# Kernel tuning notes

Hardware: AMD Instinct MI355X
Metric: run time of the kernel (lower is better)

Reference implementation:

```python
import jax, jax.numpy as jnp
import numpy as np

N_ART = 50000
N_COMM = 50000
F_IN = 768
PROJ = 1024
HID = 256
OUT = 128


def _sage(x_src, x_dst, ei, Wl, bl, Wr):
    # PyG SAGEConv (aggr='mean', root_weight=True): lin_l(mean_j x_j) + lin_r(x_dst)
    src, dst = ei[0], ei[1]
    n_dst = x_dst.shape[0]
    msg = x_src[src]                                   # [E, d_src] gather
    agg = jax.ops.segment_sum(msg, dst, num_segments=n_dst)
    cnt = jax.ops.segment_sum(jnp.ones((ei.shape[1],), x_src.dtype), dst, num_segments=n_dst)
    mean = agg / jnp.maximum(cnt, 1.0)[:, None]
    return mean @ Wl + bl + x_dst @ Wr


def setup_inputs() -> dict:
    key = jax.random.key(0)
    ks = jax.random.split(key, 22)
    w = lambda k, s: (jax.random.normal(k, s, jnp.float32) * 0.02)
    inp = {
        "article_x": jax.random.normal(ks[0], (N_ART, F_IN), jnp.float32),
        "community_x": jax.random.normal(ks[1], (N_COMM, F_IN), jnp.float32),
        "e_wb": jax.random.randint(ks[2], (2, 200000), 0, N_COMM, jnp.int32),
        "e_mb": jax.random.randint(ks[3], (2, 200000), 0, N_COMM, jnp.int32),
        "e_int": jax.random.randint(ks[4], (2, 500000), 0, N_COMM, jnp.int32),
        # lin1 / lin2 projections (F_IN -> PROJ)
        "W1": w(ks[5], (F_IN, PROJ)), "b1": jnp.zeros((PROJ,), jnp.float32),
        "W2": w(ks[6], (F_IN, PROJ)), "b2": jnp.zeros((PROJ,), jnp.float32),
        # conv1: src dim PROJ, dst dim PROJ -> HID
        "Wl1": w(ks[7], (PROJ, HID)), "bl1": jnp.zeros((HID,), jnp.float32), "Wr1": w(ks[8], (PROJ, HID)),
        # conv2: src dim PROJ, dst dim HID -> HID
        "Wl2": w(ks[9], (PROJ, HID)), "bl2": jnp.zeros((HID,), jnp.float32), "Wr2": w(ks[10], (HID, HID)),
        # conv3: src dim HID, dst dim F_IN (raw community.x) -> HID
        "Wl3": w(ks[11], (HID, HID)), "bl3": jnp.zeros((HID,), jnp.float32), "Wr3": w(ks[12], (F_IN, HID)),
        # lin3: HID -> OUT
        "W3": w(ks[13], (HID, OUT)), "b3": jnp.zeros((OUT,), jnp.float32),
    }
    return inp


def reference(article_x, community_x, e_wb, e_mb, e_int,
              W1, b1, W2, b2,
              Wl1, bl1, Wr1, Wl2, bl2, Wr2, Wl3, bl3, Wr3,
              W3, b3):
    ax = article_x @ W1 + b1          # [N_art, PROJ]
    cx = community_x @ W2 + b2        # [N_comm, PROJ]
    h1 = jax.nn.relu(_sage(ax, cx, e_wb, Wl1, bl1, Wr1))            # [N_comm, HID]
    h2 = jax.nn.relu(_sage(ax, h1, e_mb, Wl2, bl2, Wr2))            # [N_comm, HID]
    h3 = jax.nn.relu(_sage(h2, community_x, e_int, Wl3, bl3, Wr3))  # [N_comm, HID]
    return h3 @ W3 + b3               # [N_comm, OUT]
```

## Files before the change

### kernel.cpp

```cpp
#include <hip/hip_runtime.h>
#include <hip/hip_bf16.h>

#define N_NODES 50000
#define M_PAD   50048
#define MT_     391
#define F_IN    768
#define PROJ    1024
#define HID     256
#define OUTD    128
#define E_WB    200000
#define E_MB    200000
#define E_INT   500000

typedef float f32x4 __attribute__((ext_vector_type(4)));
typedef __bf16 bf16x8 __attribute__((ext_vector_type(8)));

__device__ __forceinline__ float bf2f(unsigned short u) {
  union { unsigned int i; float f; } x; x.i = ((unsigned int)u) << 16; return x.f;
}
__device__ __forceinline__ unsigned short f2bf(float f) {
  union { float f; unsigned int i; } x; x.f = f;
  unsigned int r = x.i + 0x7fff + ((x.i >> 16) & 1);
  return (unsigned short)(r >> 16);
}

__device__ __forceinline__ void gl_lds16(const void* g, void* l) {
  __builtin_amdgcn_global_load_lds((const __attribute__((address_space(1))) void*)g,
                                   (__attribute__((address_space(3))) void*)l, 16, 0, 0);
}

__global__ void bias_prep_kernel(const float* __restrict__ b1, const float* __restrict__ b2,
                                 const float* __restrict__ bl1,
                                 const float* __restrict__ Wl1, const float* __restrict__ Wl2,
                                 const float* __restrict__ Wr1,
                                 float* __restrict__ gb1, float* __restrict__ gb2,
                                 float* __restrict__ bv1) {
  int j = threadIdx.x;
  int out = blockIdx.x >> 3;
  int pg = blockIdx.x & 7;
  const float* vb = (out == 2) ? b2 : b1;
  const float* W = (out == 0) ? Wl1 : (out == 1 ? Wl2 : Wr1);
  float s = 0.f;
  int p0 = pg * 128;
#pragma unroll 4
  for (int p = p0; p < p0 + 128; ++p) s += vb[p] * W[p * HID + j];
  if (out == 2 && pg == 0) s += bl1[j];
  float* dst = (out == 0) ? gb1 : (out == 1 ? gb2 : bv1);
  atomicAdd(&dst[j], s);
}

__global__ void tcast_kernel(const float* __restrict__ src, unsigned short* __restrict__ dst,
                             int R, int C) {
  __shared__ float tile[32][33];
  int x = blockIdx.x * 32 + threadIdx.x;
  int y0 = blockIdx.y * 32;
  for (int i = threadIdx.y; i < 32; i += blockDim.y)
    tile[i][threadIdx.x] = src[(long long)(y0 + i) * C + x];
  __syncthreads();
  int xo = blockIdx.y * 32 + threadIdx.x;
  int yo0 = blockIdx.x * 32;
  for (int i = threadIdx.y; i < 32; i += blockDim.y)
    dst[(long long)(yo0 + i) * R + xo] = f2bf(tile[threadIdx.x][i]);
}

__global__ void cast_pad_kernel(const float* __restrict__ src, unsigned short* __restrict__ dst,
                                int rows_valid, long long total_chunks, int cpr) {
  long long i = (long long)blockIdx.x * 256 + threadIdx.x;
  if (i >= total_chunks) return;
  int row = (int)(i / cpr);
  int c8 = (int)(i % cpr);
  uint4 o;
  if (row < rows_valid) {
    const float4* s4 = (const float4*)src;
    long long base = (long long)row * (cpr * 2) + c8 * 2;
    float4 a = s4[base], b = s4[base + 1];
    o.x = (unsigned int)f2bf(a.x) | ((unsigned int)f2bf(a.y) << 16);
    o.y = (unsigned int)f2bf(a.z) | ((unsigned int)f2bf(a.w) << 16);
    o.z = (unsigned int)f2bf(b.x) | ((unsigned int)f2bf(b.y) << 16);
    o.w = (unsigned int)f2bf(b.z) | ((unsigned int)f2bf(b.w) << 16);
  } else {
    o.x = o.y = o.z = o.w = 0u;
  }
  ((uint4*)dst)[i] = o;
}

__global__ void count_all_kernel(const int* __restrict__ dwb, const int* __restrict__ dmb,
                                 const int* __restrict__ dint,
                                 int* __restrict__ cwb, int* __restrict__ cmb,
                                 int* __restrict__ cint) {
  int i = blockIdx.x * blockDim.x + threadIdx.x;
  const int total = E_WB + E_MB + E_INT;
  if (i >= total) return;
  if (i < E_WB) atomicAdd(&cwb[dwb[i]], 1);
  else if (i < E_WB + E_MB) atomicAdd(&cmb[dmb[i - E_WB]], 1);
  else atomicAdd(&cint[dint[i - E_WB - E_MB]], 1);
}

__global__ void scan3_kernel(const int* __restrict__ c0, const int* __restrict__ c1,
                             const int* __restrict__ c2,
                             int* __restrict__ o0, int* __restrict__ o1, int* __restrict__ o2) {
  const int* cnt = blockIdx.x == 0 ? c0 : (blockIdx.x == 1 ? c1 : c2);
  int* off = blockIdx.x == 0 ? o0 : (blockIdx.x == 1 ? o1 : o2);
  const int n = N_NODES;
  __shared__ int part[1024];
  int t = threadIdx.x;
  const int chunk = (n + 1023) / 1024;
  int lo = t * chunk, hi = lo + chunk; if (hi > n) hi = n; if (lo > n) lo = n;
  int s = 0;
  for (int i = lo; i < hi; ++i) s += cnt[i];
  part[t] = s; __syncthreads();
  for (int d = 1; d < 1024; d <<= 1) {
    int v = part[t];
    if (t >= d) v += part[t - d];
    __syncthreads();
    part[t] = v;
    __syncthreads();
  }
  int run = (t == 0) ? 0 : part[t - 1];
  for (int i = lo; i < hi; ++i) { off[i] = run; run += cnt[i]; }
  if (t == 1023) off[n] = part[1023];
}

__global__ void fill_all_kernel(const int* __restrict__ ewb, const int* __restrict__ emb,
                                const int* __restrict__ eint,
                                const int* __restrict__ owb, const int* __restrict__ omb,
                                const int* __restrict__ oint,
                                int* __restrict__ curwb, int* __restrict__ curmb,
                                int* __restrict__ curint,
                                int* __restrict__ swb, int* __restrict__ smb,
                                int* __restrict__ sint) {
  int i = blockIdx.x * blockDim.x + threadIdx.x;
  const int total = E_WB + E_MB + E_INT;
  if (i >= total) return;
  if (i < E_WB) {
    int s = ewb[i], d = ewb[E_WB + i];
    int p = atomicAdd(&curwb[d], 1);
    swb[owb[d] + p] = s;
  } else if (i < E_WB + E_MB) {
    int e = i - E_WB;
    int s = emb[e], d = emb[E_MB + e];
    int p = atomicAdd(&curmb[d], 1);
    smb[omb[d] + p] = s;
  } else {
    int e = i - E_WB - E_MB;
    int s = eint[e], d = eint[E_INT + e];
    int p = atomicAdd(&curint[d], 1);
    sint[oint[d] + p] = s;
  }
}

template <int EPI>
__global__ void __launch_bounds__(256, 2)
gemm_bt_kernel(const unsigned short* __restrict__ A, const unsigned short* __restrict__ BT,
               void* __restrict__ Cv, int K, int N, int Mvalid,
               const float* __restrict__ bias, const unsigned short* __restrict__ addm,
               int addm_stride) {
  __shared__ __align__(16) unsigned short lA[128 * 32];
  __shared__ __align__(16) unsigned short lB[128 * 32];
  const int tid = threadIdx.x;
  const int lane = tid & 63;
  const int wave = tid >> 6;
  const int NT = N >> 7;
  const int mt = blockIdx.x / NT;
  const int nt = blockIdx.x % NT;
  const int m0 = mt * 128, n0 = nt * 128;
  const int wm = (wave & 1) * 64, wn = (wave >> 1) * 64;

  f32x4 acc[4][4];
#pragma unroll
  for (int i = 0; i < 4; ++i)
#pragma unroll
    for (int j = 0; j < 4; ++j)
#pragma unroll
      for (int r = 0; r < 4; ++r) acc[i][j][r] = 0.f;

  const int r0 = tid >> 2;
  const int c0 = (tid & 3) * 8;
  const uint4* A4 = (const uint4*)A;
  const uint4* B4 = (const uint4*)BT;
  const int K8 = K >> 3;
  const int mrow = lane & 15, kq = lane >> 4;
  unsigned short* lAw = &lA[wave * 512];
  unsigned short* lBw = &lB[wave * 512];

  for (int kt = 0; kt < K; kt += 32) {
    const int kc = (kt + c0) >> 3;
    __syncthreads();
    gl_lds16(&A4[(long long)(m0 + r0) * K8 + kc], lAw);
    gl_lds16(&A4[(long long)(m0 + 64 + r0) * K8 + kc], lAw + 2048);
    gl_lds16(&B4[(long long)(n0 + r0) * K8 + kc], lBw);
    gl_lds16(&B4[(long long)(n0 + 64 + r0) * K8 + kc], lBw + 2048);
    __syncthreads();
    bf16x8 af[4], bfr[4];
#pragma unroll
    for (int i = 0; i < 4; ++i) af[i] = *(const bf16x8*)&lA[(wm + i * 16 + mrow) * 32 + kq * 8];
#pragma unroll
    for (int j = 0; j < 4; ++j) bfr[j] = *(const bf16x8*)&lB[(wn + j * 16 + mrow) * 32 + kq * 8];
#pragma unroll
    for (int i = 0; i < 4; ++i)
#pragma unroll
      for (int j = 0; j < 4; ++j)
        acc[i][j] = __builtin_amdgcn_mfma_f32_16x16x32_bf16(af[i], bfr[j], acc[i][j], 0, 0, 0);
  }

  const int col_l = lane & 15, rq = lane >> 4;
#pragma unroll
  for (int i = 0; i < 4; ++i) {
#pragma unroll
    for (int j = 0; j < 4; ++j) {
#pragma unroll
      for (int r = 0; r < 4; ++r) {
        int R = m0 + wm + i * 16 + rq * 4 + r;
        int Cc = n0 + wn + j * 16 + col_l;
        if (R < Mvalid) {
          float v = acc[i][j][r];
          if constexpr (EPI == 0) {
            ((unsigned short*)Cv)[(long long)R * N + Cc] = f2bf(v);
          } else if constexpr (EPI == 1) {
            v += bias[Cc] + bf2f(addm[(long long)R * addm_stride + Cc]);
            v = v > 0.f ? v : 0.f;
            ((unsigned short*)Cv)[(long long)R * N + Cc] = f2bf(v);
          } else {
            ((float*)Cv)[(long long)R * N + Cc] = v + bias[Cc];
          }
        }
      }
    }
  }
}

template <int MODE>
__global__ void agg_kernel(const unsigned short* __restrict__ S, int s_stride,
                           const int* __restrict__ off, const int* __restrict__ srcl,
                           const float* __restrict__ gb, const float* __restrict__ bvec,
                           const unsigned short* __restrict__ addm, int a_stride,
                           unsigned short* __restrict__ out) {
  int d = blockIdx.x;
  int c = threadIdx.x * 4;
  if (d >= N_NODES) {
    ushort4 z; z.x = z.y = z.z = z.w = 0;
    *(ushort4*)&out[(long long)d * HID + c] = z;
    return;
  }
  int lo = off[d], hi = off[d + 1];
  float s0 = 0.f, s1 = 0.f, s2 = 0.f, s3 = 0.f;
  for (int i = lo; i < hi; ++i) {
    int sidx = srcl[i];
    uint2 v = *(const uint2*)&S[(long long)sidx * s_stride + c];
    s0 += bf2f((unsigned short)(v.x & 0xffff));
    s1 += bf2f((unsigned short)(v.x >> 16));
    s2 += bf2f((unsigned short)(v.y & 0xffff));
    s3 += bf2f((unsigned short)(v.y >> 16));
  }
  int deg = hi - lo;
  float inv = deg > 0 ? 1.f / (float)deg : 0.f;
  float v0 = s0 * inv, v1 = s1 * inv, v2 = s2 * inv, v3 = s3 * inv;
  if constexpr (MODE != 2) {
    float g = deg > 0 ? 1.f : 0.f;
    uint2 am = *(const uint2*)&addm[(long long)d * a_stride + c];
    v0 += g * gb[c] + bvec[c] + bf2f((unsigned short)(am.x & 0xffff));
    v1 += g * gb[c + 1] + bvec[c + 1] + bf2f((unsigned short)(am.x >> 16));
    v2 += g * gb[c + 2] + bvec[c + 2] + bf2f((unsigned short)(am.y & 0xffff));
    v3 += g * gb[c + 3] + bvec[c + 3] + bf2f((unsigned short)(am.y >> 16));
    v0 = fmaxf(v0, 0.f); v1 = fmaxf(v1, 0.f); v2 = fmaxf(v2, 0.f); v3 = fmaxf(v3, 0.f);
  }
  ushort4 o;
  o.x = f2bf(v0); o.y = f2bf(v1); o.z = f2bf(v2); o.w = f2bf(v3);
  *(ushort4*)&out[(long long)d * HID + c] = o;
}

extern "C" void kernel_launch(void* const* d_in, const int* in_sizes, int n_in,
                              void* d_out, int out_size, void* d_ws, size_t ws_size,
                              hipStream_t stream) {
  const float* article_x = (const float*)d_in[0];
  const float* community_x = (const float*)d_in[1];
  const int* e_wb = (const int*)d_in[2];
  const int* e_mb = (const int*)d_in[3];
  const int* e_int = (const int*)d_in[4];
  const float* W1 = (const float*)d_in[5];
  const float* b1 = (const float*)d_in[6];
  const float* W2 = (const float*)d_in[7];
  const float* b2 = (const float*)d_in[8];
  const float* Wl1 = (const float*)d_in[9];
  const float* bl1 = (const float*)d_in[10];
  const float* Wr1 = (const float*)d_in[11];
  const float* Wl2 = (const float*)d_in[12];
  const float* bl2 = (const float*)d_in[13];
  const float* Wr2 = (const float*)d_in[14];
  const float* Wl3 = (const float*)d_in[15];
  const float* bl3 = (const float*)d_in[16];
  const float* Wr3 = (const float*)d_in[17];
  const float* W3 = (const float*)d_in[18];
  const float* b3 = (const float*)d_in[19];

  char* base = (char*)d_ws;
  size_t off = 0;
  auto alloc = [&](size_t bytes) -> void* {
    void* r = base + off;
    off += (bytes + 255) & ~(size_t)255;
    return r;
  };

  unsigned short* Xa = (unsigned short*)alloc((size_t)M_PAD * F_IN * 2);
  unsigned short* Xc = (unsigned short*)alloc((size_t)M_PAD * F_IN * 2);
  unsigned short* AP = (unsigned short*)alloc((size_t)M_PAD * 512 * 2);
  unsigned short* CR = (unsigned short*)alloc((size_t)M_PAD * 512 * 2);
  unsigned short* h1bf = (unsigned short*)alloc((size_t)M_PAD * HID * 2);
  unsigned short* HR2 = (unsigned short*)alloc((size_t)M_PAD * HID * 2);
  unsigned short* h2bf = (unsigned short*)alloc((size_t)M_PAD * HID * 2);
  unsigned short* mean3bf = (unsigned short*)alloc((size_t)M_PAD * HID * 2);
  unsigned short* h3bf = (unsigned short*)alloc((size_t)M_PAD * HID * 2);
  unsigned short* W1bf = (unsigned short*)alloc((size_t)F_IN * PROJ * 2);
  unsigned short* W2bf = (unsigned short*)alloc((size_t)F_IN * PROJ * 2);
  unsigned short* WlT = (unsigned short*)alloc((size_t)512 * PROJ * 2);
  unsigned short* Wr1T = (unsigned short*)alloc((size_t)HID * PROJ * 2);
  unsigned short* F12T = (unsigned short*)alloc((size_t)512 * F_IN * 2);
  unsigned short* GT = (unsigned short*)alloc((size_t)512 * F_IN * 2);
  unsigned short* Wr2T = (unsigned short*)alloc((size_t)HID * HID * 2);
  unsigned short* Wl3T = (unsigned short*)alloc((size_t)HID * HID * 2);
  unsigned short* W3T = (unsigned short*)alloc((size_t)OUTD * HID * 2);
  float* gb1 = (float*)alloc(HID * 4);
  float* gb2 = (float*)alloc(HID * 4);
  float* bv1 = (float*)alloc(HID * 4);
  int* ints_base = (int*)alloc((size_t)6 * N_NODES * 4);
  int* cnt_wb = ints_base;
  int* cur_wb = ints_base + N_NODES;
  int* cnt_mb = ints_base + 2 * N_NODES;
  int* cur_mb = ints_base + 3 * N_NODES;
  int* cnt_int = ints_base + 4 * N_NODES;
  int* cur_int = ints_base + 5 * N_NODES;
  int* off_wb = (int*)alloc((size_t)(N_NODES + 1) * 4);
  int* off_mb = (int*)alloc((size_t)(N_NODES + 1) * 4);
  int* off_int = (int*)alloc((size_t)(N_NODES + 1) * 4);
  int* srcl_wb = (int*)alloc((size_t)E_WB * 4);
  int* srcl_mb = (int*)alloc((size_t)E_MB * 4);
  int* srcl_int = (int*)alloc((size_t)E_INT * 4);

  hipMemsetAsync(ints_base, 0, (size_t)6 * N_NODES * 4, stream);
  hipMemsetAsync(gb1, 0, 3 * 1024, stream);

  cast_pad_kernel<<<(F_IN * PROJ / 8 + 255) / 256, 256, 0, stream>>>(W1, W1bf, F_IN, F_IN * (PROJ / 8), PROJ / 8);
  cast_pad_kernel<<<(F_IN * PROJ / 8 + 255) / 256, 256, 0, stream>>>(W2, W2bf, F_IN, F_IN * (PROJ / 8), PROJ / 8);
  tcast_kernel<<<dim3(HID / 32, PROJ / 32), dim3(32, 8), 0, stream>>>(Wl1, WlT, PROJ, HID);
  tcast_kernel<<<dim3(HID / 32, PROJ / 32), dim3(32, 8), 0, stream>>>(Wl2, WlT + 256 * PROJ, PROJ, HID);
  tcast_kernel<<<dim3(HID / 32, PROJ / 32), dim3(32, 8), 0, stream>>>(Wr1, Wr1T, PROJ, HID);
  tcast_kernel<<<dim3(HID / 32, F_IN / 32), dim3(32, 8), 0, stream>>>(Wr3, GT + 256 * F_IN, F_IN, HID);
  tcast_kernel<<<dim3(8, 8), dim3(32, 8), 0, stream>>>(Wr2, Wr2T, HID, HID);
  tcast_kernel<<<dim3(8, 8), dim3(32, 8), 0, stream>>>(Wl3, Wl3T, HID, HID);
  tcast_kernel<<<dim3(4, 8), dim3(32, 8), 0, stream>>>(W3, W3T, HID, OUTD);
  bias_prep_kernel<<<24, 256, 0, stream>>>(b1, b2, bl1, Wl1, Wl2, Wr1, gb1, gb2, bv1);

  gemm_bt_kernel<0><<<4 * 6, 256, 0, stream>>>(WlT, W1bf, F12T, PROJ, F_IN, 512, nullptr, nullptr, 0);
  gemm_bt_kernel<0><<<2 * 6, 256, 0, stream>>>(Wr1T, W2bf, GT, PROJ, F_IN, 256, nullptr, nullptr, 0);

  long long tc = (long long)M_PAD * (F_IN / 8);
  cast_pad_kernel<<<(unsigned)((tc + 255) / 256), 256, 0, stream>>>(article_x, Xa, N_NODES, tc, F_IN / 8);
  cast_pad_kernel<<<(unsigned)((tc + 255) / 256), 256, 0, stream>>>(community_x, Xc, N_NODES, tc, F_IN / 8);

  const int etot = E_WB + E_MB + E_INT;
  count_all_kernel<<<(etot + 255) / 256, 256, 0, stream>>>(e_wb + E_WB, e_mb + E_MB, e_int + E_INT,
                                                           cnt_wb, cnt_mb, cnt_int);
  scan3_kernel<<<3, 1024, 0, stream>>>(cnt_wb, cnt_mb, cnt_int, off_wb, off_mb, off_int);
  fill_all_kernel<<<(etot + 255) / 256, 256, 0, stream>>>(e_wb, e_mb, e_int, off_wb, off_mb, off_int,
                                                          cur_wb, cur_mb, cur_int,
                                                          srcl_wb, srcl_mb, srcl_int);

  gemm_bt_kernel<0><<<MT_ * 4, 256, 0, stream>>>(Xa, F12T, AP, F_IN, 512, N_NODES, nullptr, nullptr, 0);
  gemm_bt_kernel<0><<<MT_ * 4, 256, 0, stream>>>(Xc, GT, CR, F_IN, 512, N_NODES, nullptr, nullptr, 0);

  agg_kernel<0><<<M_PAD, 64, 0, stream>>>(AP, 512, off_wb, srcl_wb, gb1, bv1, CR, 512, h1bf);

  gemm_bt_kernel<0><<<MT_ * 2, 256, 0, stream>>>(h1bf, Wr2T, HR2, HID, HID, N_NODES, nullptr, nullptr, 0);
  agg_kernel<1><<<M_PAD, 64, 0, stream>>>(AP + 256, 512, off_mb, srcl_mb, gb2, bl2, HR2, 256, h2bf);

  agg_kernel<2><<<M_PAD, 64, 0, stream>>>(h2bf, 256, off_int, srcl_int, nullptr, nullptr, nullptr, 0, mean3bf);
  gemm_bt_kernel<1><<<MT_ * 2, 256, 0, stream>>>(mean3bf, Wl3T, h3bf, HID, HID, N_NODES, bl3, CR + 256, 512);

  gemm_bt_kernel<2><<<MT_ * 1, 256, 0, stream>>>(h3bf, W3T, d_out, HID, OUTD, N_NODES, b3, nullptr, 0);

  (void)in_sizes; (void)n_in; (void)out_size; (void)ws_size;
}
```

Before: 935.3 us.

## Merge prep kernels, batch node GEMMs, double K-step per barrier, pack agg blocks

Merges the many weight cast, transpose and bias-prep launches into one prep kernel, and folds both node feature casts into a single launch. The two weight-folding GEMMs and the two big node projection GEMMs are each batched into one launch by picking the B matrix per M tile, and the memsets are combined. The GEMM now stages two 32-wide K slices per barrier pair (64 K per iteration), which halves synchronisation but doubles LDS use. The aggregation kernels pack four destination nodes per 256-thread block instead of one per 64-thread block.

```diff
diff --git a/kernel.cpp b/kernel.cpp
--- a/kernel.cpp
+++ b/kernel.cpp
@@ -11,6 +11,7 @@
 #define E_WB    200000
 #define E_MB    200000
 #define E_INT   500000
+#define BIGM    (1 << 30)
 
 typedef float f32x4 __attribute__((ext_vector_type(4)));
 typedef __bf16 bf16x8 __attribute__((ext_vector_type(8)));
@@ -29,15 +30,66 @@
                                    (__attribute__((address_space(3))) void*)l, 16, 0, 0);
 }
 
-__global__ void bias_prep_kernel(const float* __restrict__ b1, const float* __restrict__ b2,
-                                 const float* __restrict__ bl1,
-                                 const float* __restrict__ Wl1, const float* __restrict__ Wl2,
-                                 const float* __restrict__ Wr1,
-                                 float* __restrict__ gb1, float* __restrict__ gb2,
-                                 float* __restrict__ bv1) {
+__device__ __forceinline__ void dev_cast8(const float* __restrict__ src,
+                                          unsigned short* __restrict__ dst, int blk) {
+  int i = blk * 256 + threadIdx.x;
+  const float4* s4 = (const float4*)src;
+  float4 a = s4[(long long)i * 2], b = s4[(long long)i * 2 + 1];
+  uint4 o;
+  o.x = (unsigned int)f2bf(a.x) | ((unsigned int)f2bf(a.y) << 16);
+  o.y = (unsigned int)f2bf(a.z) | ((unsigned int)f2bf(a.w) << 16);
+  o.z = (unsigned int)f2bf(b.x) | ((unsigned int)f2bf(b.y) << 16);
+  o.w = (unsigned int)f2bf(b.z) | ((unsigned int)f2bf(b.w) << 16);
+  ((uint4*)dst)[i] = o;
+}
+
+__device__ __forceinline__ void dev_tcast(const float* __restrict__ src,
+                                          unsigned short* __restrict__ dst,
+                                          int R, int C, int blk, float (*tile)[33]) {
+  int bx = blk % (C / 32), by = blk / (C / 32);
+  int tx = threadIdx.x & 31, ty = threadIdx.x >> 5;
+  int x = bx * 32 + tx, y0 = by * 32;
+  for (int i = ty; i < 32; i += 8) tile[i][tx] = src[(long long)(y0 + i) * C + x];
+  __syncthreads();
+  int xo = by * 32 + tx, yo0 = bx * 32;
+  for (int i = ty; i < 32; i += 8) dst[(long long)(yo0 + i) * R + xo] = f2bf(tile[tx][i]);
+}
+
+__global__ void prep_all_kernel(const float* __restrict__ W1, const float* __restrict__ W2,
+                                const float* __restrict__ Wl1, const float* __restrict__ Wl2,
+                                const float* __restrict__ Wr1, const float* __restrict__ Wr2,
+                                const float* __restrict__ Wl3, const float* __restrict__ Wr3,
+                                const float* __restrict__ W3,
+                                const float* __restrict__ b1, const float* __restrict__ b2,
+                                const float* __restrict__ bl1,
+                                unsigned short* __restrict__ W1bf, unsigned short* __restrict__ W2bf,
+                                unsigned short* __restrict__ WlT, unsigned short* __restrict__ Wr1T,
+                                unsigned short* __restrict__ GT_wr3, unsigned short* __restrict__ Wr2T,
+                                unsigned short* __restrict__ Wl3T, unsigned short* __restrict__ W3T,
+                                float* __restrict__ gb1, float* __restrict__ gb2,
+                                float* __restrict__ bv1) {
+  __shared__ float tile[32][33];
+  int b = blockIdx.x;
+  if (b < 384) { dev_cast8(W1, W1bf, b); return; }
+  b -= 384;
+  if (b < 384) { dev_cast8(W2, W2bf, b); return; }
+  b -= 384;
+  if (b < 256) { dev_tcast(Wl1, WlT, PROJ, HID, b, tile); return; }
+  b -= 256;
+  if (b < 256) { dev_tcast(Wl2, WlT + 256 * PROJ, PROJ, HID, b, tile); return; }
+  b -= 256;
+  if (b < 256) { dev_tcast(Wr1, Wr1T, PROJ, HID, b, tile); return; }
+  b -= 256;
+  if (b < 192) { dev_tcast(Wr3, GT_wr3, F_IN, HID, b, tile); return; }
+  b -= 192;
+  if (b < 64) { dev_tcast(Wr2, Wr2T, HID, HID, b, tile); return; }
+  b -= 64;
+  if (b < 64) { dev_tcast(Wl3, Wl3T, HID, HID, b, tile); return; }
+  b -= 64;
+  if (b < 32) { dev_tcast(W3, W3T, HID, OUTD, b, tile); return; }
+  b -= 32;
   int j = threadIdx.x;
-  int out = blockIdx.x >> 3;
-  int pg = blockIdx.x & 7;
+  int out = b >> 3, pg = b & 7;
   const float* vb = (out == 2) ? b2 : b1;
   const float* W = (out == 0) ? Wl1 : (out == 1 ? Wl2 : Wr1);
   float s = 0.f;
@@ -49,35 +101,22 @@
   atomicAdd(&dst[j], s);
 }
 
-__global__ void tcast_kernel(const float* __restrict__ src, unsigned short* __restrict__ dst,
-                             int R, int C) {
-  __shared__ float tile[32][33];
-  int x = blockIdx.x * 32 + threadIdx.x;
-  int y0 = blockIdx.y * 32;
-  for (int i = threadIdx.y; i < 32; i += blockDim.y)
-    tile[i][threadIdx.x] = src[(long long)(y0 + i) * C + x];
-  __syncthreads();
-  int xo = blockIdx.y * 32 + threadIdx.x;
-  int yo0 = blockIdx.x * 32;
-  for (int i = threadIdx.y; i < 32; i += blockDim.y)
-    dst[(long long)(yo0 + i) * R + xo] = f2bf(tile[threadIdx.x][i]);
-}
-
-__global__ void cast_pad_kernel(const float* __restrict__ src, unsigned short* __restrict__ dst,
-                                int rows_valid, long long total_chunks, int cpr) {
-  long long i = (long long)blockIdx.x * 256 + threadIdx.x;
-  if (i >= total_chunks) return;
-  int row = (int)(i / cpr);
-  int c8 = (int)(i % cpr);
+__global__ void cast_nodes_kernel(const float* __restrict__ ax, const float* __restrict__ cx,
+                                  unsigned short* __restrict__ dst) {
+  int i = blockIdx.x * 256 + threadIdx.x;
+  int row = i / 96, c8 = i % 96;
+  const float* src = ax;
+  int vrow = row;
+  if (row >= M_PAD) { src = cx; vrow = row - M_PAD; }
   uint4 o;
-  if (row < rows_valid) {
+  if (vrow < N_NODES) {
     const float4* s4 = (const float4*)src;
-    long long base = (long long)row * (cpr * 2) + c8 * 2;
-    float4 a = s4[base], b = s4[base + 1];
+    long long base = (long long)vrow * 192 + c8 * 2;
+    float4 a = s4[base], bq = s4[base + 1];
     o.x = (unsigned int)f2bf(a.x) | ((unsigned int)f2bf(a.y) << 16);
     o.y = (unsigned int)f2bf(a.z) | ((unsigned int)f2bf(a.w) << 16);
-    o.z = (unsigned int)f2bf(b.x) | ((unsigned int)f2bf(b.y) << 16);
-    o.w = (unsigned int)f2bf(b.z) | ((unsigned int)f2bf(b.w) << 16);
+    o.z = (unsigned int)f2bf(bq.x) | ((unsigned int)f2bf(bq.y) << 16);
+    o.w = (unsigned int)f2bf(bq.z) | ((unsigned int)f2bf(bq.w) << 16);
   } else {
     o.x = o.y = o.z = o.w = 0u;
   }
@@ -151,12 +190,13 @@
 
 template <int EPI>
 __global__ void __launch_bounds__(256, 2)
-gemm_bt_kernel(const unsigned short* __restrict__ A, const unsigned short* __restrict__ BT,
-               void* __restrict__ Cv, int K, int N, int Mvalid,
+gemm_bt_kernel(const unsigned short* __restrict__ A, const unsigned short* __restrict__ BT0,
+               const unsigned short* __restrict__ BT1, int mt_split,
+               void* __restrict__ Cv, int K, int N, int Mhalf, int Mvalid,
                const float* __restrict__ bias, const unsigned short* __restrict__ addm,
                int addm_stride) {
-  __shared__ __align__(16) unsigned short lA[128 * 32];
-  __shared__ __align__(16) unsigned short lB[128 * 32];
+  __shared__ __align__(16) unsigned short lA[2 * 4096];
+  __shared__ __align__(16) unsigned short lB[2 * 4096];
   const int tid = threadIdx.x;
   const int lane = tid & 63;
   const int wave = tid >> 6;
@@ -165,6 +205,7 @@
   const int nt = blockIdx.x % NT;
   const int m0 = mt * 128, n0 = nt * 128;
   const int wm = (wave & 1) * 64, wn = (wave >> 1) * 64;
+  const unsigned short* BT = (mt < mt_split) ? BT0 : BT1;
 
   f32x4 acc[4][4];
 #pragma unroll
@@ -180,27 +221,35 @@
   const uint4* B4 = (const uint4*)BT;
   const int K8 = K >> 3;
   const int mrow = lane & 15, kq = lane >> 4;
-  unsigned short* lAw = &lA[wave * 512];
-  unsigned short* lBw = &lB[wave * 512];
-
-  for (int kt = 0; kt < K; kt += 32) {
-    const int kc = (kt + c0) >> 3;
+
+  for (int kt = 0; kt < K; kt += 64) {
     __syncthreads();
-    gl_lds16(&A4[(long long)(m0 + r0) * K8 + kc], lAw);
-    gl_lds16(&A4[(long long)(m0 + 64 + r0) * K8 + kc], lAw + 2048);
-    gl_lds16(&B4[(long long)(n0 + r0) * K8 + kc], lBw);
-    gl_lds16(&B4[(long long)(n0 + 64 + r0) * K8 + kc], lBw + 2048);
+#pragma unroll
+    for (int s = 0; s < 2; ++s) {
+      const int kc = (kt + s * 32 + c0) >> 3;
+      unsigned short* lAw = &lA[s * 4096 + wave * 512];
+      unsigned short* lBw = &lB[s * 4096 + wave * 512];
+      gl_lds16(&A4[(long long)(m0 + r0) * K8 + kc], lAw);
+      gl_lds16(&A4[(long long)(m0 + 64 + r0) * K8 + kc], lAw + 2048);
+      gl_lds16(&B4[(long long)(n0 + r0) * K8 + kc], lBw);
+      gl_lds16(&B4[(long long)(n0 + 64 + r0) * K8 + kc], lBw + 2048);
+    }
     __syncthreads();
-    bf16x8 af[4], bfr[4];
-#pragma unroll
-    for (int i = 0; i < 4; ++i) af[i] = *(const bf16x8*)&lA[(wm + i * 16 + mrow) * 32 + kq * 8];
-#pragma unroll
-    for (int j = 0; j < 4; ++j) bfr[j] = *(const bf16x8*)&lB[(wn + j * 16 + mrow) * 32 + kq * 8];
-#pragma unroll
-    for (int i = 0; i < 4; ++i)
+#pragma unroll
+    for (int s = 0; s < 2; ++s) {
+      bf16x8 af[4], bfr[4];
+#pragma unroll
+      for (int i = 0; i < 4; ++i)
+        af[i] = *(const bf16x8*)&lA[s * 4096 + (wm + i * 16 + mrow) * 32 + kq * 8];
 #pragma unroll
       for (int j = 0; j < 4; ++j)
-        acc[i][j] = __builtin_amdgcn_mfma_f32_16x16x32_bf16(af[i], bfr[j], acc[i][j], 0, 0, 0);
+        bfr[j] = *(const bf16x8*)&lB[s * 4096 + (wn + j * 16 + mrow) * 32 + kq * 8];
+#pragma unroll
+      for (int i = 0; i < 4; ++i)
+#pragma unroll
+        for (int j = 0; j < 4; ++j)
+          acc[i][j] = __builtin_amdgcn_mfma_f32_16x16x32_bf16(af[i], bfr[j], acc[i][j], 0, 0, 0);
+    }
   }
 
   const int col_l = lane & 15, rq = lane >> 4;
@@ -212,7 +261,8 @@
       for (int r = 0; r < 4; ++r) {
         int R = m0 + wm + i * 16 + rq * 4 + r;
         int Cc = n0 + wn + j * 16 + col_l;
-        if (R < Mvalid) {
+        int vr = (R >= Mhalf) ? R - Mhalf : R;
+        if (vr < Mvalid) {
           float v = acc[i][j][r];
           if constexpr (EPI == 0) {
             ((unsigned short*)Cv)[(long long)R * N + Cc] = f2bf(v);
@@ -235,8 +285,8 @@
                            const float* __restrict__ gb, const float* __restrict__ bvec,
                            const unsigned short* __restrict__ addm, int a_stride,
                            unsigned short* __restrict__ out) {
-  int d = blockIdx.x;
-  int c = threadIdx.x * 4;
+  int d = blockIdx.x * 4 + (threadIdx.x >> 6);
+  int c = (threadIdx.x & 63) * 4;
   if (d >= N_NODES) {
     ushort4 z; z.x = z.y = z.z = z.w = 0;
     *(ushort4*)&out[(long long)d * HID + c] = z;
@@ -301,10 +351,9 @@
     return r;
   };
 
-  unsigned short* Xa = (unsigned short*)alloc((size_t)M_PAD * F_IN * 2);
-  unsigned short* Xc = (unsigned short*)alloc((size_t)M_PAD * F_IN * 2);
-  unsigned short* AP = (unsigned short*)alloc((size_t)M_PAD * 512 * 2);
-  unsigned short* CR = (unsigned short*)alloc((size_t)M_PAD * 512 * 2);
+  unsigned short* Xs = (unsigned short*)alloc((size_t)2 * M_PAD * F_IN * 2);
+  unsigned short* AP = (unsigned short*)alloc((size_t)2 * M_PAD * 512 * 2);
+  unsigned short* CR = AP + (size_t)M_PAD * 512;
   unsigned short* h1bf = (unsigned short*)alloc((size_t)M_PAD * HID * 2);
   unsigned short* HR2 = (unsigned short*)alloc((size_t)M_PAD * HID * 2);
   unsigned short* h2bf = (unsigned short*)alloc((size_t)M_PAD * HID * 2);
@@ -319,10 +368,10 @@
   unsigned short* Wr2T = (unsigned short*)alloc((size_t)HID * HID * 2);
   unsigned short* Wl3T = (unsigned short*)alloc((size_t)HID * HID * 2);
   unsigned short* W3T = (unsigned short*)alloc((size_t)OUTD * HID * 2);
+  int* ints_base = (int*)alloc((size_t)6 * N_NODES * 4);
   float* gb1 = (float*)alloc(HID * 4);
   float* gb2 = (float*)alloc(HID * 4);
   float* bv1 = (float*)alloc(HID * 4);
-  int* ints_base = (int*)alloc((size_t)6 * N_NODES * 4);
   int* cnt_wb = ints_base;
   int* cur_wb = ints_base + N_NODES;
   int* cnt_mb = ints_base + 2 * N_NODES;
@@ -336,26 +385,15 @@
   int* srcl_mb = (int*)alloc((size_t)E_MB * 4);
   int* srcl_int = (int*)alloc((size_t)E_INT * 4);
 
-  hipMemsetAsync(ints_base, 0, (size_t)6 * N_NODES * 4, stream);
-  hipMemsetAsync(gb1, 0, 3 * 1024, stream);
-
-  cast_pad_kernel<<<(F_IN * PROJ / 8 + 255) / 256, 256, 0, stream>>>(W1, W1bf, F_IN, F_IN * (PROJ / 8), PROJ / 8);
-  cast_pad_kernel<<<(F_IN * PROJ / 8 + 255) / 256, 256, 0, stream>>>(W2, W2bf, F_IN, F_IN * (PROJ / 8), PROJ / 8);
-  tcast_kernel<<<dim3(HID / 32, PROJ / 32), dim3(32, 8), 0, stream>>>(Wl1, WlT, PROJ, HID);
-  tcast_kernel<<<dim3(HID / 32, PROJ / 32), dim3(32, 8), 0, stream>>>(Wl2, WlT + 256 * PROJ, PROJ, HID);
-  tcast_kernel<<<dim3(HID / 32, PROJ / 32), dim3(32, 8), 0, stream>>>(Wr1, Wr1T, PROJ, HID);
-  tcast_kernel<<<dim3(HID / 32, F_IN / 32), dim3(32, 8), 0, stream>>>(Wr3, GT + 256 * F_IN, F_IN, HID);
-  tcast_kernel<<<dim3(8, 8), dim3(32, 8), 0, stream>>>(Wr2, Wr2T, HID, HID);
-  tcast_kernel<<<dim3(8, 8), dim3(32, 8), 0, stream>>>(Wl3, Wl3T, HID, HID);
-  tcast_kernel<<<dim3(4, 8), dim3(32, 8), 0, stream>>>(W3, W3T, HID, OUTD);
-  bias_prep_kernel<<<24, 256, 0, stream>>>(b1, b2, bl1, Wl1, Wl2, Wr1, gb1, gb2, bv1);
-
-  gemm_bt_kernel<0><<<4 * 6, 256, 0, stream>>>(WlT, W1bf, F12T, PROJ, F_IN, 512, nullptr, nullptr, 0);
-  gemm_bt_kernel<0><<<2 * 6, 256, 0, stream>>>(Wr1T, W2bf, GT, PROJ, F_IN, 256, nullptr, nullptr, 0);
-
-  long long tc = (long long)M_PAD * (F_IN / 8);
-  cast_pad_kernel<<<(unsigned)((tc + 255) / 256), 256, 0, stream>>>(article_x, Xa, N_NODES, tc, F_IN / 8);
-  cast_pad_kernel<<<(unsigned)((tc + 255) / 256), 256, 0, stream>>>(community_x, Xc, N_NODES, tc, F_IN / 8);
+  size_t zbytes = (size_t)((char*)bv1 + HID * 4 - (char*)ints_base);
+  hipMemsetAsync(ints_base, 0, zbytes, stream);
+
+  prep_all_kernel<<<1912, 256, 0, stream>>>(W1, W2, Wl1, Wl2, Wr1, Wr2, Wl3, Wr3, W3,
+                                            b1, b2, bl1,
+                                            W1bf, W2bf, WlT, Wr1T, GT + 256 * F_IN,
+                                            Wr2T, Wl3T, W3T, gb1, gb2, bv1);
+
+  cast_nodes_kernel<<<2 * M_PAD * 96 / 256, 256, 0, stream>>>(article_x, community_x, Xs);
 
   const int etot = E_WB + E_MB + E_INT;
   count_all_kernel<<<(etot + 255) / 256, 256, 0, stream>>>(e_wb + E_WB, e_mb + E_MB, e_int + E_INT,
@@ -365,18 +403,25 @@
                                                           cur_wb, cur_mb, cur_int,
                                                           srcl_wb, srcl_mb, srcl_int);
 
-  gemm_bt_kernel<0><<<MT_ * 4, 256, 0, stream>>>(Xa, F12T, AP, F_IN, 512, N_NODES, nullptr, nullptr, 0);
-  gemm_bt_kernel<0><<<MT_ * 4, 256, 0, stream>>>(Xc, GT, CR, F_IN, 512, N_NODES, nullptr, nullptr, 0);
-
-  agg_kernel<0><<<M_PAD, 64, 0, stream>>>(AP, 512, off_wb, srcl_wb, gb1, bv1, CR, 512, h1bf);
-
-  gemm_bt_kernel<0><<<MT_ * 2, 256, 0, stream>>>(h1bf, Wr2T, HR2, HID, HID, N_NODES, nullptr, nullptr, 0);
-  agg_kernel<1><<<M_PAD, 64, 0, stream>>>(AP + 256, 512, off_mb, srcl_mb, gb2, bl2, HR2, 256, h2bf);
-
-  agg_kernel<2><<<M_PAD, 64, 0, stream>>>(h2bf, 256, off_int, srcl_int, nullptr, nullptr, nullptr, 0, mean3bf);
-  gemm_bt_kernel<1><<<MT_ * 2, 256, 0, stream>>>(mean3bf, Wl3T, h3bf, HID, HID, N_NODES, bl3, CR + 256, 512);
-
-  gemm_bt_kernel<2><<<MT_ * 1, 256, 0, stream>>>(h3bf, W3T, d_out, HID, OUTD, N_NODES, b3, nullptr, 0);
+  gemm_bt_kernel<0><<<6 * 6, 256, 0, stream>>>(WlT, W1bf, W2bf, 4, F12T, PROJ, F_IN,
+                                               BIGM, F_IN, nullptr, nullptr, 0);
+
+  gemm_bt_kernel<0><<<2 * MT_ * 4, 256, 0, stream>>>(Xs, F12T, GT, MT_, AP, F_IN, 512,
+                                                     M_PAD, N_NODES, nullptr, nullptr, 0);
+
+  agg_kernel<0><<<M_PAD / 4, 256, 0, stream>>>(AP, 512, off_wb, srcl_wb, gb1, bv1, CR, 512, h1bf);
+
+  gemm_bt_kernel<0><<<MT_ * 2, 256, 0, stream>>>(h1bf, Wr2T, nullptr, BIGM, HR2, HID, HID,
+                                                 BIGM, N_NODES, nullptr, nullptr, 0);
+  agg_kernel<1><<<M_PAD / 4, 256, 0, stream>>>(AP + 256, 512, off_mb, srcl_mb, gb2, bl2, HR2, 256, h2bf);
+
+  agg_kernel<2><<<M_PAD / 4, 256, 0, stream>>>(h2bf, 256, off_int, srcl_int, nullptr, nullptr,
+                                               nullptr, 0, mean3bf);
+  gemm_bt_kernel<1><<<MT_ * 2, 256, 0, stream>>>(mean3bf, Wl3T, nullptr, BIGM, h3bf, HID, HID,
+                                                 BIGM, N_NODES, bl3, CR + 256, 512);
+
+  gemm_bt_kernel<2><<<MT_, 256, 0, stream>>>(h3bf, W3T, nullptr, BIGM, d_out, HID, OUTD,
+                                             BIGM, N_NODES, b3, nullptr, 0);
 
   (void)in_sizes; (void)n_in; (void)out_size; (void)ws_size;
 }
```

After: 908.5 us. 1.03x faster.
